# Optimization experiments

Measured on AMD Instinct MI355X. Metric: run time of the kernel, lower is better.

## Reference

```python
import jax, jax.numpy as jnp
import numpy as np

N = 32; D = 1152; HEADS = 16; HD = D // HEADS; DEPTH = 12
C = 4; GS = 16; P = GS * GS; PL = 16; FE = 256; NC = 1000; MLPD = 4 * D
L = C + P; SCALE = HD ** -0.5


def _ln(x, g, b):
    m = x.mean(-1, keepdims=True)
    v = ((x - m) ** 2).mean(-1, keepdims=True)
    return (x - m) * jax.lax.rsqrt(v + 1e-5) * g + b


def _sincos_pos_embed(dim, gs):
    def _1d(ed, pos):
        omega = 1.0 / 10000 ** (np.arange(ed // 2, dtype=np.float64) / (ed / 2.0))
        out = np.einsum('m,d->md', pos.reshape(-1), omega)
        return np.concatenate([np.sin(out), np.cos(out)], axis=1)
    gw, gh = np.meshgrid(np.arange(gs, dtype=np.float32), np.arange(gs, dtype=np.float32))
    return np.concatenate([_1d(dim // 2, gw), _1d(dim // 2, gh)], axis=1)


def setup_inputs():
    key = jax.random.key(0)
    ks = iter(jax.random.split(key, 64))
    r = lambda *s: 0.02 * jax.random.normal(next(ks), s, dtype=jnp.float32)
    inp = {}
    inp['x'] = jax.random.normal(next(ks), (N, P, PL), dtype=jnp.float32)
    inp['t'] = jax.random.uniform(next(ks), (N,), dtype=jnp.float32) * 1000.0
    inp['y'] = jax.random.randint(next(ks), (N,), 0, NC)
    inp['xw'] = r(PL, D); inp['xb'] = r(D)
    inp['tw1'] = r(FE, D); inp['tb1'] = r(D)
    inp['tw2'] = r(D, D); inp['tb2'] = r(D)
    inp['ytab'] = r(NC + 1, D * C)
    inp['pos'] = jnp.asarray(_sincos_pos_embed(D, GS)[None], dtype=jnp.float32)
    inp['cpos'] = r(1, C, D)
    inp['ln1g'] = 1.0 + r(DEPTH, D); inp['ln1b'] = r(DEPTH, D)
    inp['qkvw'] = r(DEPTH, D, 3 * D)
    inp['qng'] = 1.0 + r(DEPTH, HD); inp['qnb'] = r(DEPTH, HD)
    inp['kng'] = 1.0 + r(DEPTH, HD); inp['knb'] = r(DEPTH, HD)
    inp['pw'] = r(DEPTH, D, D); inp['pb'] = r(DEPTH, D)
    inp['ln2g'] = 1.0 + r(DEPTH, D); inp['ln2b'] = r(DEPTH, D)
    inp['f1w'] = r(DEPTH, D, MLPD); inp['f1b'] = r(DEPTH, MLPD)
    inp['f2w'] = r(DEPTH, MLPD, D); inp['f2b'] = r(DEPTH, D)
    inp['fng'] = 1.0 + r(D); inp['fnb'] = r(D)
    inp['ow'] = r(D, PL); inp['ob'] = r(PL)
    return inp


def reference(x, t, y, xw, xb, tw1, tb1, tw2, tb2, ytab, pos, cpos,
              ln1g, ln1b, qkvw, qng, qnb, kng, knb, pw, pb,
              ln2g, ln2b, f1w, f1b, f2w, f2b, fng, fnb, ow, ob):
    n = x.shape[0]
    # timestep embedding (sinusoidal -> MLP with SiLU)
    half = FE // 2
    freqs = jnp.exp(-jnp.log(jnp.float32(10000.0)) * jnp.arange(half, dtype=jnp.float32) / half)
    a = t[:, None] * freqs[None]
    temb = jnp.concatenate([jnp.cos(a), jnp.sin(a)], axis=-1)  # [N, FE]
    temb = jax.nn.silu(temb @ tw1 + tb1) @ tw2 + tb2           # [N, D]
    # label embedding -> num_cond_tokens conditioning tokens (eval: no label drop)
    cond = ytab[y].reshape(n, C, D) + cpos + temb[:, None, :]  # [N, C, D]
    # patch token projection + fixed sincos pos embed
    xt = x @ xw + xb + pos                                     # [N, P, D]
    tok = jnp.concatenate([cond, xt], axis=1)                  # [N, L, D]
    mask = jnp.triu(jnp.ones((L, L), dtype=bool), k=1)         # causal (True = masked)

    def block(tok, p):
        g1, b1, qw, qg, qb, kg, kb, pww, pbb, g2, b2, w1, bb1, w2, bb2 = p
        h = _ln(tok, g1, b1)
        qkv = (h @ qw).reshape(n, L, 3, HEADS, HD).transpose(2, 0, 3, 1, 4)
        q, k, v = qkv[0], qkv[1], qkv[2]                       # [N, H, L, HD]
        q = _ln(q, qg, qb) * SCALE
        k = _ln(k, kg, kb)
        att = jnp.einsum('nhqd,nhkd->nhqk', q, k)
        att = jnp.where(mask, jnp.float32(-1e9), att)
        att = jax.nn.softmax(att, axis=-1)
        o = jnp.einsum('nhqk,nhkd->nhqd', att, v).transpose(0, 2, 1, 3).reshape(n, L, D)
        tok = tok + (o @ pww + pbb)
        h2 = _ln(tok, g2, b2)
        tok = tok + (jax.nn.gelu(h2 @ w1 + bb1, approximate=True) @ w2 + bb2)
        return tok, None

    tok, _ = jax.lax.scan(block, tok,
                          (ln1g, ln1b, qkvw, qng, qnb, kng, knb, pw, pb,
                           ln2g, ln2b, f1w, f1b, f2w, f2b))
    out = _ln(tok, fng, fnb) @ ow + ob                          # [N, L, PL]
    return out[:, C:]                                           # predictions for patch tokens
```

## Files before the change

### kernel.cpp

```cpp
#include <hip/hip_runtime.h>
#include <hip/hip_bf16.h>
#include <cstdint>

#define DEV __device__ __forceinline__

typedef __attribute__((ext_vector_type(8))) short bf16x8;
typedef __attribute__((ext_vector_type(4))) float f32x4;
typedef unsigned short u16;
typedef unsigned int u32;

constexpr int BN_   = 32;
constexpr int PP    = 256;
constexpr int PL_   = 16;
constexpr int CT    = 4;
constexpr int LL    = 260;
constexpr int DD    = 1152;
constexpr int HH    = 16;
constexpr int HDIM  = 72;
constexpr int DEPTH_= 12;
constexpr int TD    = 3456;
constexpr int MLPD_ = 4608;
constexpr int MREAL = BN_*LL;
constexpr int MPAD  = 8448;
constexpr int LP    = 288;
constexpr int HDP   = 96;
constexpr int HDV   = 80;
constexpr float SCALE_ = 0.11785113019775793f;

constexpr size_t OP_ = (size_t)TD*DD;
constexpr size_t OF1 = OP_ + (size_t)DD*DD;
constexpr size_t OF2 = OF1 + (size_t)MLPD_*DD;
constexpr size_t ARENA_ELEMS = OF2 + (size_t)1280*MLPD_;

DEV u16 f2bf(float f){
    union{float f; u32 i;} c; c.f = f;
    u32 u = c.i;
    u32 r = (u + 0x7fffu + ((u>>16)&1u)) >> 16;
    return (u16)r;
}
DEV float bf2f(u32 u){ union{u32 i; float f;} c; c.i = u<<16; return c.f; }

DEV float wave_sum64(float v){
    #pragma unroll
    for (int off=32; off; off>>=1) v += __shfl_xor(v, off);
    return v;
}
DEV float group16_sum(float v){
    #pragma unroll
    for (int off=8; off; off>>=1) v += __shfl_xor(v, off);
    return v;
}
DEV float gelu_f(float x){
    float u = 0.7978845608028654f * (x + 0.044715f * x*x*x);
    return x / (1.f + __expf(-2.f * u));
}

__global__ void temb1_kernel(const float* __restrict__ t, const float* __restrict__ tw1,
                             const float* __restrict__ tb1, float* __restrict__ e1)
{
    int n = blockIdx.y, j = blockIdx.x*128 + threadIdx.x;
    float tv = t[n];
    float acc = tb1[j];
    const float k = 0.07195578415606394f;
    for (int i = 0; i < 128; ++i) {
        float f = __expf(-k * (float)i);
        float a = tv * f;
        float sa = sinf(a), ca = cosf(a);
        acc += ca * tw1[(size_t)i*DD + j] + sa * tw1[(size_t)(i+128)*DD + j];
    }
    e1[(size_t)n*DD + j] = acc / (1.f + __expf(-acc));
}

__global__ void temb2_kernel(const float* __restrict__ e1, const float* __restrict__ tw2,
                             const float* __restrict__ tb2, float* __restrict__ te)
{
    int n = blockIdx.y, j = blockIdx.x*128 + threadIdx.x;
    float acc = tb2[j];
    const float* er = e1 + (size_t)n*DD;
    for (int kk = 0; kk < DD; ++kk)
        acc += er[kk] * tw2[(size_t)kk*DD + j];
    te[(size_t)n*DD + j] = acc;
}

__global__ void assemble_kernel(const float* __restrict__ x, const int* __restrict__ y,
                                const float* __restrict__ xw, const float* __restrict__ xb,
                                const float* __restrict__ ytab, const float* __restrict__ pos,
                                const float* __restrict__ cpos, const float* __restrict__ te,
                                float* __restrict__ tokf)
{
    int m = blockIdx.x;
    if (m >= MREAL) {
        for (int d = threadIdx.x; d < DD; d += 256) tokf[(size_t)m*DD + d] = 0.f;
        return;
    }
    int n = m / LL, l = m % LL;
    if (l < CT) {
        int cls = y[n];
        const float* yt = ytab + (size_t)cls*(CT*DD) + (size_t)l*DD;
        const float* cp = cpos + (size_t)l*DD;
        const float* tm = te + (size_t)n*DD;
        for (int d = threadIdx.x; d < DD; d += 256)
            tokf[(size_t)m*DD + d] = yt[d] + cp[d] + tm[d];
    } else {
        int p = l - CT;
        const float* xr = x + (size_t)(n*PP + p)*PL_;
        float xv[16];
        #pragma unroll
        for (int i=0;i<16;i++) xv[i] = xr[i];
        const float* pr = pos + (size_t)p*DD;
        for (int d = threadIdx.x; d < DD; d += 256) {
            float acc = xb[d] + pr[d];
            #pragma unroll
            for (int i=0;i<16;i++) acc += xv[i] * xw[(size_t)i*DD + d];
            tokf[(size_t)m*DD + d] = acc;
        }
    }
}

__global__ void convln_kernel(const float* __restrict__ qkvw, const float* __restrict__ pw,
                              const float* __restrict__ f1w, const float* __restrict__ f2w,
                              u16* __restrict__ arena,
                              const float* __restrict__ src, const float* __restrict__ g,
                              const float* __restrict__ b, u16* __restrict__ dst)
{
    __shared__ float tile[64][65];
    int id = blockIdx.x;
    if (id >= 3888) {
        int lane = threadIdx.x & 63, w = threadIdx.x >> 6;
        int m = (id - 3888)*4 + w;
        const float* row = src + (size_t)m * DD;
        float4 v[5];
        float s = 0.f, ss = 0.f;
        #pragma unroll
        for (int i=0;i<5;i++) {
            int idx = i*64 + lane;
            if (idx < 288) {
                v[i] = ((const float4*)row)[idx];
                s  += v[i].x + v[i].y + v[i].z + v[i].w;
                ss += v[i].x*v[i].x + v[i].y*v[i].y + v[i].z*v[i].z + v[i].w*v[i].w;
            }
        }
        s = wave_sum64(s); ss = wave_sum64(ss);
        float mean = s * (1.f/DD);
        float var  = ss * (1.f/DD) - mean*mean;
        float rs   = rsqrtf(var + 1e-5f);
        u16* orow = dst + (size_t)m*DD;
        #pragma unroll
        for (int i=0;i<5;i++) {
            int idx = i*64 + lane;
            if (idx < 288) {
                int c0 = idx*4;
                float4 gg = ((const float4*)g)[idx];
                float4 bb = ((const float4*)b)[idx];
                ushort4 o;
                o.x = f2bf((v[i].x-mean)*rs*gg.x + bb.x);
                o.y = f2bf((v[i].y-mean)*rs*gg.y + bb.y);
                o.z = f2bf((v[i].z-mean)*rs*gg.z + bb.z);
                o.w = f2bf((v[i].w-mean)*rs*gg.w + bb.w);
                *(ushort4*)(orow + c0) = o;
            }
        }
        return;
    }
    const float* W; u16* WT; int K, Nw, t0;
    if (id < 972)        { W = qkvw; WT = arena;        K = DD;    Nw = TD;    t0 = id; }
    else if (id < 1296)  { W = pw;   WT = arena + OP_;  K = DD;    Nw = DD;    t0 = id - 972; }
    else if (id < 2592)  { W = f1w;  WT = arena + OF1;  K = DD;    Nw = MLPD_; t0 = id - 1296; }
    else                 { W = f2w;  WT = arena + OF2;  K = MLPD_; Nw = DD;    t0 = id - 2592; }
    int nx = Nw >> 6;
    int nb = (t0 % nx) * 64, kb = (t0 / nx) * 64;
    int tx = threadIdx.x & 63, ty = threadIdx.x >> 6;
    #pragma unroll
    for (int r=0;r<16;r++)
        tile[r*4 + ty][tx] = W[(size_t)(kb + r*4 + ty)*Nw + nb + tx];
    __syncthreads();
    int j = threadIdx.x & 63, i2 = threadIdx.x >> 6;
    #pragma unroll
    for (int r=0;r<16;r++) {
        int n = i2 + r*4;
        WT[(size_t)(nb + n)*K + kb + j] = f2bf(tile[j][n]);
    }
}

__global__ void ln_kernel(const float* __restrict__ src, const float* __restrict__ g,
                          const float* __restrict__ b, u16* __restrict__ dst)
{
    int lane = threadIdx.x & 63, w = threadIdx.x >> 6;
    int m = blockIdx.x*4 + w;
    const float* row = src + (size_t)m * DD;
    float4 v[5];
    float s = 0.f, ss = 0.f;
    #pragma unroll
    for (int i=0;i<5;i++) {
        int idx = i*64 + lane;
        if (idx < 288) {
            v[i] = ((const float4*)row)[idx];
            s  += v[i].x + v[i].y + v[i].z + v[i].w;
            ss += v[i].x*v[i].x + v[i].y*v[i].y + v[i].z*v[i].z + v[i].w*v[i].w;
        }
    }
    s = wave_sum64(s); ss = wave_sum64(ss);
    float mean = s * (1.f/DD);
    float var  = ss * (1.f/DD) - mean*mean;
    float rs   = rsqrtf(var + 1e-5f);
    u16* orow = dst + (size_t)m*DD;
    #pragma unroll
    for (int i=0;i<5;i++) {
        int idx = i*64 + lane;
        if (idx < 288) {
            int c0 = idx*4;
            float4 gg = ((const float4*)g)[idx];
            float4 bb = ((const float4*)b)[idx];
            ushort4 o;
            o.x = f2bf((v[i].x-mean)*rs*gg.x + bb.x);
            o.y = f2bf((v[i].y-mean)*rs*gg.y + bb.y);
            o.z = f2bf((v[i].z-mean)*rs*gg.z + bb.z);
            o.w = f2bf((v[i].w-mean)*rs*gg.w + bb.w);
            *(ushort4*)(orow + c0) = o;
        }
    }
}

template<int EPI>
__global__ __launch_bounds__(256, 4)
void gemm97_kernel(const u16* __restrict__ A, const u16* __restrict__ BT,
                   int K, int Nreal, u16* __restrict__ outb, float* __restrict__ outf,
                   const float* __restrict__ bias)
{
    __shared__ u16 As[128][64];
    __shared__ u16 Bs[128][64];
    const int tid = threadIdx.x;
    const int lane = tid & 63, wv = tid >> 6;
    const int wq = wv >> 1, wp = wv & 1;
    const int l15 = lane & 15, g4 = lane >> 4;

    const int id = blockIdx.x + gridDim.x * blockIdx.y;
    const int total = gridDim.x * gridDim.y;
    const int qch = total >> 3, rch = total & 7;
    const int xcd = id & 7, ps = id >> 3;
    const int wg = (xcd < rch ? xcd*(qch+1) : rch*(qch+1) + (xcd-rch)*qch) + ps;
    const int m0 = (wg / gridDim.x) * 128, n0 = (wg % gridDim.x) * 128;

    const int rr = tid >> 3, chv = tid & 7;
    const int cxo = (chv ^ (rr & 7)) * 8;
    const u16* gA = A  + (size_t)(m0 + rr) * K + cxo;
    const u16* gB = BT + (size_t)(n0 + rr) * K + cxo;

    auto stageA = [&](int kk) {
        #pragma unroll
        for (int i=0;i<4;i++)
            __builtin_amdgcn_global_load_lds(
                (const __attribute__((address_space(1))) void*)(gA + (size_t)(i*32)*K + kk),
                (__attribute__((address_space(3))) void*)(&As[i*32 + wv*8][0]), 16, 0, 0);
    };
    auto stageB = [&](int kk) {
        #pragma unroll
        for (int i=0;i<4;i++)
            __builtin_amdgcn_global_load_lds(
                (const __attribute__((address_space(1))) void*)(gB + (size_t)(i*32)*K + kk),
                (__attribute__((address_space(3))) void*)(&Bs[i*32 + wv*8][0]), 16, 0, 0);
    };
    auto rdA = [&](int m, int ks)->bf16x8 {
        int r = wq*64 + m*16 + l15;
        return *(const bf16x8*)(&As[r][((ks*4 + g4) ^ (r & 7))*8]);
    };
    auto rdB = [&](int n, int ks)->bf16x8 {
        int r = wp*64 + n*16 + l15;
        return *(const bf16x8*)(&Bs[r][((ks*4 + g4) ^ (r & 7))*8]);
    };

    f32x4 acc[4][4];
    #pragma unroll
    for (int i=0;i<4;i++)
        #pragma unroll
        for (int j=0;j<4;j++) acc[i][j] = (f32x4){0.f,0.f,0.f,0.f};

    const int NT = K >> 6;
    for (int t = 0; t < NT; ++t) {
        stageA(t << 6); stageB(t << 6);
        __syncthreads();
        #pragma unroll
        for (int ks=0; ks<2; ++ks) {
            bf16x8 aF[4], bF[4];
            #pragma unroll
            for (int m=0;m<4;m++) aF[m] = rdA(m, ks);
            #pragma unroll
            for (int n=0;n<4;n++) bF[n] = rdB(n, ks);
            #pragma unroll
            for (int m=0;m<4;m++)
                #pragma unroll
                for (int n=0;n<4;n++)
                    acc[m][n] = __builtin_amdgcn_mfma_f32_16x16x32_bf16(aF[m], bF[n], acc[m][n], 0,0,0);
        }
        __syncthreads();
    }

    #pragma unroll
    for (int m=0;m<4;m++) {
        const int gr = m0 + wq*64 + m*16 + g4*4;
        #pragma unroll
        for (int n=0;n<4;n++) {
            const int gc = n0 + wp*64 + n*16 + l15;
            if (gc < Nreal) {
                #pragma unroll
                for (int r=0;r<4;r++) {
                    float vv = acc[m][n][r];
                    size_t oi = (size_t)(gr + r)*Nreal + gc;
                    if constexpr (EPI == 0) {
                        outb[oi] = f2bf(vv);
                    } else if constexpr (EPI == 1) {
                        outb[oi] = f2bf(gelu_f(vv + bias[gc]));
                    } else {
                        outf[oi] = outf[oi] + vv + bias[gc];
                    }
                }
            }
        }
    }
}

template<int EPI>
__global__ __launch_bounds__(512, 4)
void gemm256_kernel(const u16* __restrict__ A, const u16* __restrict__ BT,
                    int K, int Nreal, u16* __restrict__ outb,
                    const float* __restrict__ bias)
{
    __shared__ u16 As[256][64];
    __shared__ u16 Bs[128][64];
    const int tid = threadIdx.x;
    const int lane = tid & 63, wv = tid >> 6;
    const int wm = wv & 3, wn = wv >> 2;
    const int l15 = lane & 15, g4 = lane >> 4;

    const int id = blockIdx.x + gridDim.x * blockIdx.y;
    const int total = gridDim.x * gridDim.y;
    const int qch = total >> 3, rch = total & 7;
    const int xcd = id & 7, ps = id >> 3;
    const int wg = (xcd < rch ? xcd*(qch+1) : rch*(qch+1) + (xcd-rch)*qch) + ps;
    const int m0 = (wg / gridDim.x) * 256, n0 = (wg % gridDim.x) * 128;

    const int rr = tid >> 3, chv = tid & 7;
    const int cxo = (chv ^ (rr & 7)) * 8;
    const u16* gA = A  + (size_t)(m0 + rr) * K + cxo;
    const u16* gB = BT + (size_t)(n0 + rr) * K + cxo;

    auto stageA = [&](int kk) {
        #pragma unroll
        for (int i=0;i<4;i++)
            __builtin_amdgcn_global_load_lds(
                (const __attribute__((address_space(1))) void*)(gA + (size_t)(i*64)*K + kk),
                (__attribute__((address_space(3))) void*)(&As[i*64 + wv*8][0]), 16, 0, 0);
    };
    auto stageB = [&](int kk) {
        #pragma unroll
        for (int i=0;i<2;i++)
            __builtin_amdgcn_global_load_lds(
                (const __attribute__((address_space(1))) void*)(gB + (size_t)(i*64)*K + kk),
                (__attribute__((address_space(3))) void*)(&Bs[i*64 + wv*8][0]), 16, 0, 0);
    };
    auto rdA = [&](int m, int ks)->bf16x8 {
        int r = wm*64 + m*16 + l15;
        return *(const bf16x8*)(&As[r][((ks*4 + g4) ^ (r & 7))*8]);
    };
    auto rdB = [&](int n, int ks)->bf16x8 {
        int r = wn*64 + n*16 + l15;
        return *(const bf16x8*)(&Bs[r][((ks*4 + g4) ^ (r & 7))*8]);
    };

    f32x4 acc[4][4];
    #pragma unroll
    for (int i=0;i<4;i++)
        #pragma unroll
        for (int j=0;j<4;j++) acc[i][j] = (f32x4){0.f,0.f,0.f,0.f};

    const int NT = K >> 6;
    for (int t = 0; t < NT; ++t) {
        stageA(t << 6); stageB(t << 6);
        __syncthreads();
        #pragma unroll
        for (int ks=0; ks<2; ++ks) {
            bf16x8 aF[4], bF[4];
            #pragma unroll
            for (int m=0;m<4;m++) aF[m] = rdA(m, ks);
            #pragma unroll
            for (int n=0;n<4;n++) bF[n] = rdB(n, ks);
            #pragma unroll
            for (int m=0;m<4;m++)
                #pragma unroll
                for (int n=0;n<4;n++)
                    acc[m][n] = __builtin_amdgcn_mfma_f32_16x16x32_bf16(aF[m], bF[n], acc[m][n], 0,0,0);
        }
        __syncthreads();
    }

    #pragma unroll
    for (int m=0;m<4;m++) {
        const int gr = m0 + wm*64 + m*16 + g4*4;
        #pragma unroll
        for (int n=0;n<4;n++) {
            const int gc = n0 + wn*64 + n*16 + l15;
            if (gc < Nreal) {
                #pragma unroll
                for (int r=0;r<4;r++) {
                    float vv = acc[m][n][r];
                    size_t oi = (size_t)(gr + r)*Nreal + gc;
                    if constexpr (EPI == 0) {
                        outb[oi] = f2bf(vv);
                    } else {
                        outb[oi] = f2bf(gelu_f(vv + bias[gc]));
                    }
                }
            }
        }
    }
}

__global__ void qkvt_kernel(const u16* __restrict__ qkv,
                            const float* __restrict__ qg, const float* __restrict__ qb,
                            const float* __restrict__ kg, const float* __restrict__ kb,
                            u16* __restrict__ qn, u16* __restrict__ kn, u16* __restrict__ vt)
{
    __shared__ u16 tile[32][81];
    int id = blockIdx.x;
    if (id < 512) {
        int b = id; int h = b & 15, n = b >> 4;
        int tid = threadIdx.x;
        const size_t vbase = 2*DD + (size_t)h*HDIM;
        u16* vto = vt + (size_t)b * (HDV*LP);
        for (int lt = 0; lt < 9; ++lt) {
            #pragma unroll
            for (int e = 0; e < 9; ++e) {
                int ei = e*256 + tid;
                int r = ei / 72, c = ei - r*72;
                int l = lt*32 + r;
                u16 v = 0;
                if (l < LL) v = qkv[((size_t)n*LL + l)*TD + vbase + c];
                tile[r][c] = v;
            }
            __syncthreads();
            int j = tid & 31, hd0 = tid >> 5;
            #pragma unroll
            for (int e = 0; e < 10; ++e) {
                int hd = hd0 + e*8;
                u16 v = (hd < HDIM) ? tile[j][hd] : (u16)0;
                vto[(size_t)hd*LP + lt*32 + j] = v;
            }
            __syncthreads();
        }
        return;
    }
    int lane = threadIdx.x & 63, w = threadIdx.x >> 6;
    int s = lane & 15, g = lane >> 4;
    int idx = (id - 512)*16 + w*4 + g;
    int l = idx % LP; int nh = idx / LP;
    int h = nh & 15, n = nh >> 4;
    u32* qrow = (u32*)(qn + (size_t)idx * HDP);
    u32* krow = (u32*)(kn + (size_t)idx * HDP);
    if (l >= LL) {
        #pragma unroll
        for (int j=0;j<3;j++) { qrow[s + 16*j] = 0u; krow[s + 16*j] = 0u; }
        return;
    }
    size_t m = (size_t)n*LL + l;
    const u32* qs = (const u32*)(qkv + m*TD + h*HDIM);
    const u32* ks = (const u32*)(qkv + m*TD + DD + h*HDIM);

    float q0[3], q1[3], k0[3], k1[3];
    float sq = 0.f, sqq = 0.f, sk = 0.f, skk = 0.f;
    #pragma unroll
    for (int j=0;j<3;j++) {
        int c = s + 16*j;
        q0[j]=q1[j]=k0[j]=k1[j]=0.f;
        if (c < 36) {
            u32 uq = qs[c]; q0[j] = bf2f(uq & 0xffffu); q1[j] = bf2f(uq >> 16);
            u32 uk = ks[c]; k0[j] = bf2f(uk & 0xffffu); k1[j] = bf2f(uk >> 16);
        }
        sq += q0[j]+q1[j]; sqq += q0[j]*q0[j]+q1[j]*q1[j];
        sk += k0[j]+k1[j]; skk += k0[j]*k0[j]+k1[j]*k1[j];
    }
    sq = group16_sum(sq); sqq = group16_sum(sqq);
    sk = group16_sum(sk); skk = group16_sum(skk);
    float mq = sq*(1.f/HDIM), vq = sqq*(1.f/HDIM) - mq*mq, rq = rsqrtf(vq + 1e-5f);
    float mk = sk*(1.f/HDIM), vk = skk*(1.f/HDIM) - mk*mk, rk = rsqrtf(vk + 1e-5f);
    #pragma unroll
    for (int j=0;j<3;j++) {
        int c = s + 16*j;
        if (c < 36) {
            float o0 = ((q0[j]-mq)*rq*qg[c*2]   + qb[c*2]  ) * SCALE_;
            float o1 = ((q1[j]-mq)*rq*qg[c*2+1] + qb[c*2+1]) * SCALE_;
            qrow[c] = (u32)f2bf(o0) | ((u32)f2bf(o1) << 16);
            float p0 = (k0[j]-mk)*rk*kg[c*2]   + kb[c*2];
            float p1 = (k1[j]-mk)*rk*kg[c*2+1] + kb[c*2+1];
            krow[c] = (u32)f2bf(p0) | ((u32)f2bf(p1) << 16);
        } else {
            qrow[c] = 0u; krow[c] = 0u;
        }
    }
}

__global__ __launch_bounds__(256)
void attn_kernel(const u16* __restrict__ qn, const u16* __restrict__ kn,
                 const u16* __restrict__ vt, u16* __restrict__ obuf)
{
    __shared__ u16 Pl[4][512];
    int b = blockIdx.x; int h = b & 15, n = b >> 4;
    int by = blockIdx.y;
    int lane = threadIdx.x & 63, w = threadIdx.x >> 6;
    const u16* qb_ = qn + (size_t)b * (LP*HDP);
    const u16* kb_ = kn + (size_t)b * (LP*HDP);
    const u16* vb_ = vt + (size_t)b * (HDV*LP);
    const int l15 = lane & 15, g4 = lane >> 4;
    const int slot = w + 4*by;

    for (int t = slot; t < 17; t += 16) {
        int qr0 = t*16;
        bf16x8 aq[3];
        #pragma unroll
        for (int fi=0; fi<3; ++fi)
            aq[fi] = *(const bf16x8*)(qb_ + (size_t)(qr0 + l15)*HDP + fi*32 + g4*8);
        f32x4 o[5];
        #pragma unroll
        for (int ht=0; ht<5; ++ht) o[ht] = (f32x4){0.f,0.f,0.f,0.f};
        float mrow[4], ssum[4];
        #pragma unroll
        for (int r=0;r<4;r++){ mrow[r] = -1e30f; ssum[r] = 0.f; }

        int umax = (qr0 + 15) >> 5;
        for (int u = 0; u <= umax; ++u) {
            f32x4 sacc[2];
            #pragma unroll
            for (int cc=0; cc<2; ++cc) {
                sacc[cc] = (f32x4){0.f,0.f,0.f,0.f};
                #pragma unroll
                for (int fi=0; fi<3; ++fi) {
                    bf16x8 bk = *(const bf16x8*)(kb_ + (size_t)(u*32 + cc*16 + l15)*HDP + fi*32 + g4*8);
                    sacc[cc] = __builtin_amdgcn_mfma_f32_16x16x32_bf16(aq[fi], bk, sacc[cc], 0,0,0);
                }
            }
            float pv0[4], pv1[4];
            #pragma unroll
            for (int r=0;r<4;r++) {
                int qi = qr0 + g4*4 + r;
                float s0 = ((u*32 + l15)      <= qi) ? sacc[0][r] : -1e30f;
                float s1 = ((u*32 + 16 + l15) <= qi) ? sacc[1][r] : -1e30f;
                float mx = fmaxf(s0, s1);
                mx = fmaxf(mx, __shfl_xor(mx, 1));
                mx = fmaxf(mx, __shfl_xor(mx, 2));
                mx = fmaxf(mx, __shfl_xor(mx, 4));
                mx = fmaxf(mx, __shfl_xor(mx, 8));
                float nm = fmaxf(mrow[r], mx);
                float sc = __expf(mrow[r] - nm);
                float p0 = __expf(s0 - nm), p1 = __expf(s1 - nm);
                float rsm = p0 + p1;
                rsm += __shfl_xor(rsm, 1); rsm += __shfl_xor(rsm, 2);
                rsm += __shfl_xor(rsm, 4); rsm += __shfl_xor(rsm, 8);
                ssum[r] = ssum[r]*sc + rsm;
                mrow[r] = nm;
                #pragma unroll
                for (int ht=0; ht<5; ++ht) o[ht][r] *= sc;
                pv0[r] = p0; pv1[r] = p1;
            }
            u16* pw_ = Pl[w];
            #pragma unroll
            for (int r=0;r<4;r++) {
                pw_[(g4*4+r)*32 + l15]      = f2bf(pv0[r]);
                pw_[(g4*4+r)*32 + 16 + l15] = f2bf(pv1[r]);
            }
            bf16x8 aP = *(const bf16x8*)(pw_ + l15*32 + g4*8);
            #pragma unroll
            for (int ht=0; ht<5; ++ht) {
                bf16x8 bv = *(const bf16x8*)(vb_ + (size_t)(ht*16 + l15)*LP + u*32 + g4*8);
                o[ht] = __builtin_amdgcn_mfma_f32_16x16x32_bf16(aP, bv, o[ht], 0,0,0);
            }
        }
        #pragma unroll
        for (int r=0;r<4;r++) {
            int l = qr0 + g4*4 + r;
            if (l < LL) {
                float inv = 1.f / ssum[r];
                size_t mro = ((size_t)n*LL + l)*DD + (size_t)h*HDIM;
                #pragma unroll
                for (int ht=0; ht<5; ++ht) {
                    int hd = ht*16 + l15;
                    if (hd < HDIM) obuf[mro + hd] = f2bf(o[ht][r] * inv);
                }
            }
        }
    }
}

__global__ __launch_bounds__(256)
void outproj_kernel(const float* __restrict__ tokf, const float* __restrict__ g,
                    const float* __restrict__ b, const float* __restrict__ ow,
                    const float* __restrict__ ob, float* __restrict__ out)
{
    __shared__ float hrow[4][1152];
    int lane = threadIdx.x & 63, w = threadIdx.x >> 6;
    int idx = blockIdx.x*4 + w;
    int n = idx >> 8, p = idx & 255;
    size_t m = (size_t)n*LL + CT + p;
    const float* row = tokf + m*DD;
    float4 v[5];
    float s = 0.f, ss = 0.f;
    #pragma unroll
    for (int i=0;i<5;i++) {
        int id = i*64 + lane;
        if (id < 288) {
            v[i] = ((const float4*)row)[id];
            s  += v[i].x + v[i].y + v[i].z + v[i].w;
            ss += v[i].x*v[i].x + v[i].y*v[i].y + v[i].z*v[i].z + v[i].w*v[i].w;
        }
    }
    s = wave_sum64(s); ss = wave_sum64(ss);
    float mean = s*(1.f/DD), var = ss*(1.f/DD) - mean*mean;
    float rs = rsqrtf(var + 1e-5f);
    #pragma unroll
    for (int i=0;i<5;i++) {
        int id = i*64 + lane;
        if (id < 288) {
            int c0 = id*4;
            float4 gg = ((const float4*)g)[id];
            float4 bb = ((const float4*)b)[id];
            hrow[w][c0+0] = (v[i].x-mean)*rs*gg.x + bb.x;
            hrow[w][c0+1] = (v[i].y-mean)*rs*gg.y + bb.y;
            hrow[w][c0+2] = (v[i].z-mean)*rs*gg.z + bb.z;
            hrow[w][c0+3] = (v[i].w-mean)*rs*gg.w + bb.w;
        }
    }
    __syncthreads();
    int c = lane & 15, q = lane >> 4;
    float acc = 0.f;
    const float* hq = hrow[w] + q*288;
    const float* owq = ow + (size_t)(q*288)*16 + c;
    #pragma unroll 4
    for (int d = 0; d < 288; ++d)
        acc += hq[d] * owq[(size_t)d*16];
    acc += __shfl_xor(acc, 16);
    acc += __shfl_xor(acc, 32);
    if (lane < 16) {
        out[((size_t)n*PP + p)*PL_ + c] = acc + ob[c];
    }
}

extern "C" void kernel_launch(void* const* d_in, const int* in_sizes, int n_in,
                              void* d_out, int out_size, void* d_ws, size_t ws_size,
                              hipStream_t stream)
{
    const float* x    = (const float*)d_in[0];
    const float* t    = (const float*)d_in[1];
    const int*   y    = (const int*)d_in[2];
    const float* xw   = (const float*)d_in[3];
    const float* xb   = (const float*)d_in[4];
    const float* tw1  = (const float*)d_in[5];
    const float* tb1  = (const float*)d_in[6];
    const float* tw2  = (const float*)d_in[7];
    const float* tb2  = (const float*)d_in[8];
    const float* ytab = (const float*)d_in[9];
    const float* pos  = (const float*)d_in[10];
    const float* cpos = (const float*)d_in[11];
    const float* ln1g = (const float*)d_in[12];
    const float* ln1b = (const float*)d_in[13];
    const float* qkvw = (const float*)d_in[14];
    const float* qng  = (const float*)d_in[15];
    const float* qnbi = (const float*)d_in[16];
    const float* kng  = (const float*)d_in[17];
    const float* knbi = (const float*)d_in[18];
    const float* pw   = (const float*)d_in[19];
    const float* pb   = (const float*)d_in[20];
    const float* ln2g = (const float*)d_in[21];
    const float* ln2b = (const float*)d_in[22];
    const float* f1w  = (const float*)d_in[23];
    const float* f1b  = (const float*)d_in[24];
    const float* f2w  = (const float*)d_in[25];
    const float* f2b  = (const float*)d_in[26];
    const float* fng  = (const float*)d_in[27];
    const float* fnb  = (const float*)d_in[28];
    const float* ow   = (const float*)d_in[29];
    const float* ob   = (const float*)d_in[30];
    float* out = (float*)d_out;

    char* wsb = (char*)d_ws;
    size_t off = 0;
    auto alloc = [&](size_t bytes)->void* {
        void* p = wsb + off; off += (bytes + 255) & ~(size_t)255; return p;
    };
    float* tokf = (float*)alloc((size_t)MPAD*DD*4);
    u16*   hbuf = (u16*)  alloc((size_t)MPAD*DD*2);
    u16*   qkvb = (u16*)  alloc((size_t)MPAD*TD*2);
    u16*   qnb_ = (u16*)  alloc((size_t)BN_*HH*LP*HDP*2);
    u16*   knb_ = (u16*)  alloc((size_t)BN_*HH*LP*HDP*2);
    u16*   vtb  = (u16*)  alloc((size_t)BN_*HH*HDV*LP*2);
    u16*   obuf = (u16*)  alloc((size_t)MPAD*DD*2);
    u16*   mid  = (u16*)  alloc((size_t)MPAD*MLPD_*2);
    u16*   wT   = (u16*)  alloc(ARENA_ELEMS*2);
    float* e1   = (float*)alloc((size_t)BN_*DD*4);
    float* te   = (float*)alloc((size_t)BN_*DD*4);
    (void)ws_size; (void)in_sizes; (void)n_in; (void)out_size;

    temb1_kernel<<<dim3(9,32),128,0,stream>>>(t, tw1, tb1, e1);
    temb2_kernel<<<dim3(9,32),128,0,stream>>>(e1, tw2, tb2, te);
    assemble_kernel<<<MPAD,256,0,stream>>>(x, y, xw, xb, ytab, pos, cpos, te, tokf);

    for (int L_ = 0; L_ < DEPTH_; ++L_) {
        convln_kernel<<<3888 + MPAD/4,256,0,stream>>>(qkvw + (size_t)L_*DD*TD, pw + (size_t)L_*DD*DD,
                                                      f1w + (size_t)L_*DD*MLPD_, f2w + (size_t)L_*MLPD_*DD,
                                                      wT, tokf, ln1g + L_*DD, ln1b + L_*DD, hbuf);
        gemm256_kernel<0><<<dim3(27, 33),512,0,stream>>>(hbuf, wT, DD, TD, qkvb, nullptr);
        qkvt_kernel<<<512 + BN_*HH*LP/16,256,0,stream>>>(qkvb, qng + L_*HDIM, qnbi + L_*HDIM,
                                                         kng + L_*HDIM, knbi + L_*HDIM, qnb_, knb_, vtb);
        attn_kernel<<<dim3(BN_*HH, 4),256,0,stream>>>(qnb_, knb_, vtb, obuf);
        gemm97_kernel<2><<<dim3(9, 66),256,0,stream>>>(obuf, wT + OP_, DD, DD, nullptr, tokf, pb + L_*DD);
        ln_kernel<<<MPAD/4,256,0,stream>>>(tokf, ln2g + L_*DD, ln2b + L_*DD, hbuf);
        gemm256_kernel<1><<<dim3(36, 33),512,0,stream>>>(hbuf, wT + OF1, DD, MLPD_, mid, f1b + L_*MLPD_);
        gemm97_kernel<2><<<dim3(9, 66),256,0,stream>>>(mid, wT + OF2, MLPD_, DD, nullptr, tokf, f2b + L_*DD);
    }
    outproj_kernel<<<(BN_*PP)/4,256,0,stream>>>(tokf, fng, fnb, ow, ob, out);
}
```

Measured before the change: 5.724 ms.

## Overlap next-layer weight transpose with the MLP-up GEMM via double-buffered arena

Moves the per-layer fp32-to-bf16 weight transpose for layer L+1 out of the separate convln launch and into extra blocks appended to the layer L fc1 GEMM grid. The weight arena is double-buffered, and LN1 for the next layer becomes a standalone ln_kernel. The aim is to let the bandwidth-bound transpose fill idle CUs during the compute-bound GEMM and to drop a serial launch. In exchange the arena takes twice the workspace, and the transpose blocks (512 threads, 64x64 tiles) compete with the GEMM for CUs and memory bandwidth.

```diff
diff --git a/kernel.cpp b/kernel.cpp
--- a/kernel.cpp
+++ b/kernel.cpp
@@ -323,21 +323,49 @@
 __global__ __launch_bounds__(512, 4)
 void gemm256_kernel(const u16* __restrict__ A, const u16* __restrict__ BT,
                     int K, int Nreal, u16* __restrict__ outb,
-                    const float* __restrict__ bias)
+                    const float* __restrict__ bias,
+                    int nxg, int gemmBlocks,
+                    const float* __restrict__ nqkvw, const float* __restrict__ npw,
+                    const float* __restrict__ nf1w, const float* __restrict__ nf2w,
+                    u16* __restrict__ narena)
 {
     __shared__ u16 As[256][64];
     __shared__ u16 Bs[128][64];
+    const int bid = blockIdx.x;
+    if (bid >= gemmBlocks) {
+        float* tile = (float*)&As[0][0];
+        int id = bid - gemmBlocks;
+        const float* W; u16* WT; int K2, Nw, t0;
+        if (id < 972)        { W = nqkvw; WT = narena;        K2 = DD;    Nw = TD;    t0 = id; }
+        else if (id < 1296)  { W = npw;   WT = narena + OP_;  K2 = DD;    Nw = DD;    t0 = id - 972; }
+        else if (id < 2592)  { W = nf1w;  WT = narena + OF1;  K2 = DD;    Nw = MLPD_; t0 = id - 1296; }
+        else                 { W = nf2w;  WT = narena + OF2;  K2 = MLPD_; Nw = DD;    t0 = id - 2592; }
+        int nx = Nw >> 6;
+        int nb = (t0 % nx) * 64, kb = (t0 / nx) * 64;
+        int tx = threadIdx.x & 63, ty = threadIdx.x >> 6;
+        #pragma unroll
+        for (int r=0;r<8;r++)
+            tile[(r*8 + ty)*65 + tx] = W[(size_t)(kb + r*8 + ty)*Nw + nb + tx];
+        __syncthreads();
+        int j = threadIdx.x & 63, i2 = threadIdx.x >> 6;
+        #pragma unroll
+        for (int r=0;r<8;r++) {
+            int n = i2 + r*8;
+            WT[(size_t)(nb + n)*K2 + kb + j] = f2bf(tile[j*65 + n]);
+        }
+        return;
+    }
     const int tid = threadIdx.x;
     const int lane = tid & 63, wv = tid >> 6;
     const int wm = wv & 3, wn = wv >> 2;
     const int l15 = lane & 15, g4 = lane >> 4;
 
-    const int id = blockIdx.x + gridDim.x * blockIdx.y;
-    const int total = gridDim.x * gridDim.y;
+    const int id = bid;
+    const int total = gemmBlocks;
     const int qch = total >> 3, rch = total & 7;
     const int xcd = id & 7, ps = id >> 3;
     const int wg = (xcd < rch ? xcd*(qch+1) : rch*(qch+1) + (xcd-rch)*qch) + ps;
-    const int m0 = (wg / gridDim.x) * 256, n0 = (wg % gridDim.x) * 128;
+    const int m0 = (wg / nxg) * 256, n0 = (wg % nxg) * 128;
 
     const int rr = tid >> 3, chv = tid & 7;
     const int cxo = (chv ^ (rr & 7)) * 8;
@@ -692,7 +720,7 @@
     u16*   vtb  = (u16*)  alloc((size_t)BN_*HH*HDV*LP*2);
     u16*   obuf = (u16*)  alloc((size_t)MPAD*DD*2);
     u16*   mid  = (u16*)  alloc((size_t)MPAD*MLPD_*2);
-    u16*   wT   = (u16*)  alloc(ARENA_ELEMS*2);
+    u16*   wT   = (u16*)  alloc((size_t)2*ARENA_ELEMS*2);
     float* e1   = (float*)alloc((size_t)BN_*DD*4);
     float* te   = (float*)alloc((size_t)BN_*DD*4);
     (void)ws_size; (void)in_sizes; (void)n_in; (void)out_size;
@@ -701,18 +729,31 @@
     temb2_kernel<<<dim3(9,32),128,0,stream>>>(e1, tw2, tb2, te);
     assemble_kernel<<<MPAD,256,0,stream>>>(x, y, xw, xb, ytab, pos, cpos, te, tokf);
 
+    convln_kernel<<<3888 + MPAD/4,256,0,stream>>>(qkvw, pw, f1w, f2w, wT,
+                                                  tokf, ln1g, ln1b, hbuf);
+
     for (int L_ = 0; L_ < DEPTH_; ++L_) {
-        convln_kernel<<<3888 + MPAD/4,256,0,stream>>>(qkvw + (size_t)L_*DD*TD, pw + (size_t)L_*DD*DD,
-                                                      f1w + (size_t)L_*DD*MLPD_, f2w + (size_t)L_*MLPD_*DD,
-                                                      wT, tokf, ln1g + L_*DD, ln1b + L_*DD, hbuf);
-        gemm256_kernel<0><<<dim3(27, 33),512,0,stream>>>(hbuf, wT, DD, TD, qkvb, nullptr);
+        u16* wa = wT + (size_t)(L_ & 1)*ARENA_ELEMS;
+        u16* wn = wT + (size_t)((L_+1) & 1)*ARENA_ELEMS;
+        gemm256_kernel<0><<<891,512,0,stream>>>(hbuf, wa, DD, TD, qkvb, nullptr,
+                                                27, 891, nullptr, nullptr, nullptr, nullptr, nullptr);
         qkvt_kernel<<<512 + BN_*HH*LP/16,256,0,stream>>>(qkvb, qng + L_*HDIM, qnbi + L_*HDIM,
                                                          kng + L_*HDIM, knbi + L_*HDIM, qnb_, knb_, vtb);
         attn_kernel<<<dim3(BN_*HH, 4),256,0,stream>>>(qnb_, knb_, vtb, obuf);
-        gemm97_kernel<2><<<dim3(9, 66),256,0,stream>>>(obuf, wT + OP_, DD, DD, nullptr, tokf, pb + L_*DD);
+        gemm97_kernel<2><<<dim3(9, 66),256,0,stream>>>(obuf, wa + OP_, DD, DD, nullptr, tokf, pb + L_*DD);
         ln_kernel<<<MPAD/4,256,0,stream>>>(tokf, ln2g + L_*DD, ln2b + L_*DD, hbuf);
-        gemm256_kernel<1><<<dim3(36, 33),512,0,stream>>>(hbuf, wT + OF1, DD, MLPD_, mid, f1b + L_*MLPD_);
-        gemm97_kernel<2><<<dim3(9, 66),256,0,stream>>>(mid, wT + OF2, MLPD_, DD, nullptr, tokf, f2b + L_*DD);
+        if (L_ < DEPTH_-1) {
+            gemm256_kernel<1><<<1188 + 3888,512,0,stream>>>(hbuf, wa + OF1, DD, MLPD_, mid, f1b + L_*MLPD_,
+                36, 1188,
+                qkvw + (size_t)(L_+1)*DD*TD, pw + (size_t)(L_+1)*DD*DD,
+                f1w + (size_t)(L_+1)*DD*MLPD_, f2w + (size_t)(L_+1)*MLPD_*DD, wn);
+        } else {
+            gemm256_kernel<1><<<1188,512,0,stream>>>(hbuf, wa + OF1, DD, MLPD_, mid, f1b + L_*MLPD_,
+                36, 1188, nullptr, nullptr, nullptr, nullptr, nullptr);
+        }
+        gemm97_kernel<2><<<dim3(9, 66),256,0,stream>>>(mid, wa + OF2, MLPD_, DD, nullptr, tokf, f2b + L_*DD);
+        if (L_ < DEPTH_-1)
+            ln_kernel<<<MPAD/4,256,0,stream>>>(tokf, ln1g + (L_+1)*DD, ln1b + (L_+1)*DD, hbuf);
     }
     outproj_kernel<<<(BN_*PP)/4,256,0,stream>>>(tokf, fng, fnb, ow, ob, out);
 }
```

New measurement: 5.753 ms. About the same (+0.5%).
